# Kernel optimization log

Measured on AMD Instinct MI355X. Metric: run time of the kernel, lower is better.

## Reference

```python
import jax, jax.numpy as jnp
import numpy as np

NUM_HEADS = 16
NEG_INF = -1e18


def setup_inputs() -> dict:
    key = jax.random.key(0)
    ks = jax.random.split(key, 9)
    T, B, D = 2048, 2, 1024
    s = 1.0 / np.sqrt(D)
    return {
        "query": jax.random.normal(ks[0], (T, B, D), jnp.float32),
        "q_w": jax.random.normal(ks[1], (D, D), jnp.float32) * s,
        "q_b": jax.random.normal(ks[2], (D,), jnp.float32) * 0.02,
        "k_w": jax.random.normal(ks[3], (D, D), jnp.float32) * s,
        "k_b": jax.random.normal(ks[4], (D,), jnp.float32) * 0.02,
        "v_w": jax.random.normal(ks[5], (D, D), jnp.float32) * s,
        "v_b": jax.random.normal(ks[6], (D,), jnp.float32) * 0.02,
        "out_w": jax.random.normal(ks[7], (D, D), jnp.float32) * s,
        "out_b": jax.random.normal(ks[8], (D,), jnp.float32) * 0.02,
    }


def reference(query, q_w, q_b, k_w, k_b, v_w, v_b, out_w, out_b):
    # query: [T, B, D] (Time x Batch x Channel). Self-attention, causal mask,
    # dropout=0, need_weights=True.
    T, B, D = query.shape
    H = NUM_HEADS
    hd = D // H
    scaling = 1.0 / jnp.sqrt(jnp.asarray(hd, query.dtype))

    q = (query @ q_w.T + q_b) * scaling
    k = query @ k_w.T + k_b
    v = query @ v_w.T + v_b

    def split_heads(x):  # [T, B, D] -> [B, H, T, hd]
        return x.reshape(T, B, H, hd).transpose(1, 2, 0, 3)

    qh, kh, vh = split_heads(q), split_heads(k), split_heads(v)

    # scores: [B, H, T, T]
    scores = jnp.einsum("bhtd,bhsd->bhts", qh, kh)
    causal = jnp.triu(jnp.full((T, T), NEG_INF, dtype=scores.dtype), k=1)
    scores = scores + causal

    probs = jax.nn.softmax(scores, axis=-1)
    attn = jnp.einsum("bhts,bhsd->bhtd", probs, vh)  # [B, H, T, hd]
    attn = attn.transpose(2, 0, 1, 3).reshape(T, B, D)
    out = attn @ out_w.T + out_b

    # averaged attention weights over heads: [B, T, T]
    avg_weights = probs.sum(axis=1) / H
    return out, avg_weights
```

## Files before the change

### kernel.cpp

```cpp
#include <hip/hip_runtime.h>
#include <hip/hip_bf16.h>
#include <stdint.h>

typedef __hip_bfloat16 bf16;
using short8 = __attribute__((ext_vector_type(8))) short;
using f32x4  = __attribute__((ext_vector_type(4))) float;

#define TDIM 2048
#define BDIM 2
#define DDIM 1024
#define HNUM 16
#define HD   64
#define MDIM 4096
#define M0   16.0f
#define L2E  1.44269504088896f
#define M0B  23.0831207f

__device__ __forceinline__ f32x4 mfma16(short8 a, short8 b, f32x4 c) {
  return __builtin_amdgcn_mfma_f32_16x16x32_bf16(a, b, c, 0, 0, 0);
}

__device__ __forceinline__ float fexp2(float s) {
  return __builtin_amdgcn_exp2f(__builtin_fmaf(s, L2E, -M0B));
}

union S8 { short8 v; bf16 h[8]; };
union P4 { uint2 u; bf16 h[4]; };

__global__ __launch_bounds__(256) void cast_all_kernel(
    const float* __restrict__ q, const float* __restrict__ wq,
    const float* __restrict__ wk, const float* __restrict__ wv,
    const float* __restrict__ wo, bf16* __restrict__ dst) {
  int t4 = blockIdx.x * blockDim.x + threadIdx.x;
  int idx = t4 * 4;
  const float* s;
  if (idx < 4194304)      s = q  + idx;
  else if (idx < 5242880) s = wq + (idx - 4194304);
  else if (idx < 6291456) s = wk + (idx - 5242880);
  else if (idx < 7340032) s = wv + (idx - 6291456);
  else                    s = wo + (idx - 7340032);
  float4 v = *(const float4*)s;
  union { ushort4 u; bf16 b[4]; } pk;
  pk.b[0] = __float2bfloat16(v.x);
  pk.b[1] = __float2bfloat16(v.y);
  pk.b[2] = __float2bfloat16(v.z);
  pk.b[3] = __float2bfloat16(v.w);
  *(ushort4*)(dst + idx) = pk.u;
}

__global__ __launch_bounds__(256, 2) void qkv_kernel(
    const bf16* __restrict__ X, const bf16* __restrict__ Wq,
    const bf16* __restrict__ Wk, const bf16* __restrict__ Wv,
    const float* __restrict__ qb, const float* __restrict__ kb,
    const float* __restrict__ vb, bf16* __restrict__ Qo,
    bf16* __restrict__ Ko, bf16* __restrict__ Vto) {
  __shared__ __align__(16) bf16 Xs[128][72];
  __shared__ __align__(16) bf16 Qs[64][72];
  __shared__ __align__(16) bf16 Ks[64][72];
  __shared__ __align__(16) bf16 Vs[64][72];
  const int tid  = threadIdx.x;
  const int lane = tid & 63, wave = tid >> 6;
  const int m0 = blockIdx.y * 128, n0 = blockIdx.x * 64;
  const int wm = (wave >> 1) * 64, wn = (wave & 1) * 32;
  const int fr = lane & 15, quad = lane >> 4, q8 = quad * 8;
  const int r = tid >> 3, cc = (tid & 7) * 8;
  f32x4 aq[4][2] = {}, ak[4][2] = {}, av[2][4] = {};
  const bf16* xp = X  + (size_t)(m0 + r) * DDIM + cc;
  const bf16* qp = Wq + (size_t)(n0 + r) * DDIM + cc;
  const bf16* kp = Wk + (size_t)(n0 + r) * DDIM + cc;
  const bf16* vp = Wv + (size_t)(n0 + r) * DDIM + cc;
  uint4 xv0, xv1, xv2, xv3, qv0, qv1, kv0, kv1, vv0, vv1;
#define QKV_LD(K0)                                                  \
  do {                                                              \
    xv0 = *(const uint4*)(xp + (K0));                               \
    xv1 = *(const uint4*)(xp + (size_t)32 * DDIM + (K0));           \
    xv2 = *(const uint4*)(xp + (size_t)64 * DDIM + (K0));           \
    xv3 = *(const uint4*)(xp + (size_t)96 * DDIM + (K0));           \
    qv0 = *(const uint4*)(qp + (K0));                               \
    qv1 = *(const uint4*)(qp + (size_t)32 * DDIM + (K0));           \
    kv0 = *(const uint4*)(kp + (K0));                               \
    kv1 = *(const uint4*)(kp + (size_t)32 * DDIM + (K0));           \
    vv0 = *(const uint4*)(vp + (K0));                               \
    vv1 = *(const uint4*)(vp + (size_t)32 * DDIM + (K0));           \
  } while (0)
  QKV_LD(0);
  for (int k0 = 0; k0 < DDIM; k0 += 64) {
    __syncthreads();
    *(uint4*)&Xs[r][cc]      = xv0;
    *(uint4*)&Xs[r + 32][cc] = xv1;
    *(uint4*)&Xs[r + 64][cc] = xv2;
    *(uint4*)&Xs[r + 96][cc] = xv3;
    *(uint4*)&Qs[r][cc]      = qv0;
    *(uint4*)&Qs[r + 32][cc] = qv1;
    *(uint4*)&Ks[r][cc]      = kv0;
    *(uint4*)&Ks[r + 32][cc] = kv1;
    *(uint4*)&Vs[r][cc]      = vv0;
    *(uint4*)&Vs[r + 32][cc] = vv1;
    __syncthreads();
    if (k0 + 64 < DDIM) QKV_LD(k0 + 64);
#pragma unroll
    for (int kk = 0; kk < 2; kk++) {
      const int ko = kk * 32 + q8;
      short8 xf[4], qf[2], kf[2], vf[2];
#pragma unroll
      for (int i = 0; i < 4; i++)
        xf[i] = *(const short8*)&Xs[wm + i * 16 + fr][ko];
#pragma unroll
      for (int j = 0; j < 2; j++) {
        qf[j] = *(const short8*)&Qs[wn + j * 16 + fr][ko];
        kf[j] = *(const short8*)&Ks[wn + j * 16 + fr][ko];
        vf[j] = *(const short8*)&Vs[wn + j * 16 + fr][ko];
      }
#pragma unroll
      for (int i = 0; i < 4; i++)
#pragma unroll
        for (int j = 0; j < 2; j++) {
          aq[i][j] = mfma16(xf[i], qf[j], aq[i][j]);
          ak[i][j] = mfma16(xf[i], kf[j], ak[i][j]);
          av[j][i] = mfma16(vf[j], xf[i], av[j][i]);
        }
    }
  }
#undef QKV_LD
#pragma unroll
  for (int mt = 0; mt < 4; mt++)
#pragma unroll
    for (int nt = 0; nt < 2; nt++)
#pragma unroll
      for (int i = 0; i < 4; i++) {
        int gm = m0 + wm + mt * 16 + quad * 4 + i;
        int gn = n0 + wn + nt * 16 + fr;
        int t = gm >> 1, bb = gm & 1, h = gn >> 6, e = gn & 63;
        size_t o = ((size_t)(bb * HNUM + h) * TDIM + t) * HD + e;
        Qo[o] = __float2bfloat16((aq[mt][nt][i] + qb[gn]) * 0.125f);
        Ko[o] = __float2bfloat16(ak[mt][nt][i] + kb[gn]);
      }
#pragma unroll
  for (int vt = 0; vt < 2; vt++)
#pragma unroll
    for (int xt = 0; xt < 4; xt++)
#pragma unroll
      for (int i = 0; i < 4; i++) {
        int gf = n0 + wn + vt * 16 + quad * 4 + i;
        int gt = m0 + wm + xt * 16 + fr;
        int t = gt >> 1, bb = gt & 1, h = gf >> 6, e = gf & 63;
        Vto[((size_t)(bb * HNUM + h) * HD + e) * TDIM + t] =
            __float2bfloat16(av[vt][xt][i] + vb[gf]);
      }
}

__global__ __launch_bounds__(256) void gemm_out_kernel(
    const bf16* __restrict__ P0, const bf16* __restrict__ P1,
    const bf16* __restrict__ Bw, const float* __restrict__ l0buf,
    const float* __restrict__ l1buf, const float* __restrict__ bias,
    float* __restrict__ of32) {
  __shared__ __align__(16) bf16 As[64][72];
  __shared__ __align__(16) bf16 Bs[64][72];
  __shared__ float sInv[64][16];
  const int tid  = threadIdx.x;
  const int lane = tid & 63, wave = tid >> 6;
  const int m0 = blockIdx.y * 64, n0 = blockIdx.x * 64;
  const int wm = (wave >> 1) * 32, wn = (wave & 1) * 32;
  const int fr = lane & 15, quad = lane >> 4, q8 = quad * 8;
  const int ldr = tid >> 3, ldc = (tid & 7) * 8;
#pragma unroll
  for (int e = 0; e < 4; e++) {
    int idx = tid * 4 + e;
    int row = idx >> 4, h = idx & 15;
    int gm = m0 + row, t = gm >> 1, bb = gm & 1;
    size_t li = (size_t)(bb * HNUM + h) * TDIM + t;
    sInv[row][h] = 1.0f / (l0buf[li] + l1buf[li]);
  }
  f32x4 acc[2][2] = {};
  const size_t ar0 = (size_t)(m0 + ldr) * DDIM + ldc;
  const size_t ar1 = ar0 + (size_t)32 * DDIM;
  const bf16* bp0 = Bw + (size_t)(n0 + ldr) * DDIM + ldc;
  const bf16* bp1 = bp0 + (size_t)32 * DDIM;
  short8 p00v, p10v, p01v, p11v;
  uint4 bv0, bv1;
#define OUT_LD(K0)                                  \
  do {                                              \
    p00v = *(const short8*)&P0[ar0 + (K0)];         \
    p10v = *(const short8*)&P1[ar0 + (K0)];         \
    p01v = *(const short8*)&P0[ar1 + (K0)];         \
    p11v = *(const short8*)&P1[ar1 + (K0)];         \
    bv0  = *(const uint4*)(bp0 + (K0));             \
    bv1  = *(const uint4*)(bp1 + (K0));             \
  } while (0)
  OUT_LD(0);
  __syncthreads();
  for (int k0 = 0; k0 < DDIM; k0 += 64) {
    const float inv0 = sInv[ldr][k0 >> 6];
    const float inv1 = sInv[ldr + 32][k0 >> 6];
    S8 s00, s10, s01, s11, w0, w1;
    s00.v = p00v; s10.v = p10v; s01.v = p01v; s11.v = p11v;
#pragma unroll
    for (int k = 0; k < 8; k++) {
      w0.h[k] = __float2bfloat16(
          (__bfloat162float(s00.h[k]) + __bfloat162float(s10.h[k])) * inv0);
      w1.h[k] = __float2bfloat16(
          (__bfloat162float(s01.h[k]) + __bfloat162float(s11.h[k])) * inv1);
    }
    __syncthreads();
    *(short8*)&As[ldr][ldc]      = w0.v;
    *(short8*)&As[ldr + 32][ldc] = w1.v;
    *(uint4*)&Bs[ldr][ldc]       = bv0;
    *(uint4*)&Bs[ldr + 32][ldc]  = bv1;
    __syncthreads();
    if (k0 + 64 < DDIM) OUT_LD(k0 + 64);
#pragma unroll
    for (int kk = 0; kk < 2; kk++) {
      const int ko = kk * 32 + q8;
      short8 af0, af1, bf0, bf1;
      af0 = *(const short8*)&As[wm + fr][ko];
      af1 = *(const short8*)&As[wm + 16 + fr][ko];
      bf0 = *(const short8*)&Bs[wn + fr][ko];
      bf1 = *(const short8*)&Bs[wn + 16 + fr][ko];
      acc[0][0] = mfma16(af0, bf0, acc[0][0]);
      acc[0][1] = mfma16(af0, bf1, acc[0][1]);
      acc[1][0] = mfma16(af1, bf0, acc[1][0]);
      acc[1][1] = mfma16(af1, bf1, acc[1][1]);
    }
  }
#undef OUT_LD
#pragma unroll
  for (int mt = 0; mt < 2; mt++)
#pragma unroll
    for (int nt = 0; nt < 2; nt++)
#pragma unroll
      for (int i = 0; i < 4; i++) {
        int gm = m0 + wm + mt * 16 + quad * 4 + i;
        int gn = n0 + wn + nt * 16 + fr;
        of32[(size_t)gm * DDIM + gn] = acc[mt][nt][i] + bias[gn];
      }
}

__global__ __launch_bounds__(256) void attn_split_kernel(
    const bf16* __restrict__ Q, const bf16* __restrict__ K,
    const bf16* __restrict__ Vt, bf16* __restrict__ P0o,
    bf16* __restrict__ P1o, float* __restrict__ l0buf,
    float* __restrict__ l1buf) {
  __shared__ __align__(16) bf16 Ks[2][64][40];
  __shared__ __align__(16) bf16 Vs[2][64][40];
  __shared__ __align__(16) bf16 pt[4][32][72];
  const int tid = threadIdx.x, lane = tid & 63, wave = tid >> 6;
  const int bid = blockIdx.x;
  const int part = bid & 1, bh = (bid >> 1) & 31, t128 = 15 - (bid >> 6);
  const int b = bh >> 4, h = bh & 15;
  const int t0 = t128 * 128 + wave * 32;
  const int fr = lane & 15, quad = lane >> 4, q8 = quad * 8;
  const bf16* Qp = Q + ((size_t)bh * TDIM + t0) * HD;
  const bf16* Kp = K + (size_t)bh * TDIM * HD;
  const bf16* Vp = Vt + (size_t)bh * HD * TDIM;
  short8 aq[2][2];
  aq[0][0] = *(const short8*)&Qp[fr * HD + q8];
  aq[0][1] = *(const short8*)&Qp[fr * HD + 32 + q8];
  aq[1][0] = *(const short8*)&Qp[(16 + fr) * HD + q8];
  aq[1][1] = *(const short8*)&Qp[(16 + fr) * HD + 32 + q8];
  const int Cb = 2 * t128 + 2, C0 = t128 + 1;
  const int clo = part ? C0 : 0, chi = part ? Cb : C0;
  const int sr0 = tid >> 3, scc = (tid & 7) * 8, sr1 = sr0 + 32;
  const int ssub = scc >> 5, scol = scc & 31;
  f32x4 oacc[2][4] = {};
  float lsum[2] = {0.f, 0.f};
  uint4 kv0, kv1, vv0, vv1;
  auto ldglob = [&](int c) {
    int s0 = c * 64;
    kv0 = *(const uint4*)&Kp[(size_t)(s0 + sr0) * HD + scc];
    kv1 = *(const uint4*)&Kp[(size_t)(s0 + sr1) * HD + scc];
    vv0 = *(const uint4*)&Vp[(size_t)sr0 * TDIM + s0 + scc];
    vv1 = *(const uint4*)&Vp[(size_t)sr1 * TDIM + s0 + scc];
  };
  ldglob(clo);
  for (int c = clo; c < chi; c++) {
    __syncthreads();
    *(uint4*)&Ks[ssub][sr0][scol] = kv0;
    *(uint4*)&Ks[ssub][sr1][scol] = kv1;
    *(uint4*)&Vs[ssub][sr0][scol] = vv0;
    *(uint4*)&Vs[ssub][sr1][scol] = vv1;
    __syncthreads();
    if (c + 1 < chi) ldglob(c + 1);
    const int s0 = c * 64;
    if (s0 > t0 + 31) continue;
    f32x4 scT[2][4] = {};
#pragma unroll
    for (int j = 0; j < 4; j++) {
      short8 k0f = *(const short8*)&Ks[0][j * 16 + fr][q8];
      short8 k1f = *(const short8*)&Ks[1][j * 16 + fr][q8];
      scT[0][j] = mfma16(k0f, aq[0][0], scT[0][j]);
      scT[0][j] = mfma16(k1f, aq[0][1], scT[0][j]);
      scT[1][j] = mfma16(k0f, aq[1][0], scT[1][j]);
      scT[1][j] = mfma16(k1f, aq[1][1], scT[1][j]);
    }
#pragma unroll
    for (int g = 0; g < 2; g++) {
      const int tg = t0 + g * 16;
#pragma unroll
      for (int j = 0; j < 4; j++) {
        const int sj = s0 + j * 16;
        P4 pk;
        if (sj > tg + 15) {
          pk.u = make_uint2(0u, 0u);
        } else if (sj + 15 <= tg) {
#pragma unroll
          for (int i = 0; i < 4; i++) {
            float p = fexp2(scT[g][j][i]);
            lsum[g] += p;
            pk.h[i] = __float2bfloat16(p);
          }
        } else {
          const int t_row = tg + fr;
          const int s_base = sj + quad * 4;
#pragma unroll
          for (int i = 0; i < 4; i++) {
            float p = 0.f;
            if (s_base + i <= t_row) {
              p = fexp2(scT[g][j][i]);
              lsum[g] += p;
            }
            pk.h[i] = __float2bfloat16(p);
          }
        }
        *(uint2*)&pt[wave][g * 16 + fr][j * 16 + quad * 4] = pk.u;
      }
    }
#pragma unroll
    for (int c2 = 0; c2 < 2; c2++) {
      short8 ap0 = *(const short8*)&pt[wave][fr][c2 * 32 + q8];
      short8 ap1 = *(const short8*)&pt[wave][16 + fr][c2 * 32 + q8];
#pragma unroll
      for (int nt = 0; nt < 4; nt++) {
        short8 vf = *(const short8*)&Vs[c2][nt * 16 + fr][q8];
        oacc[0][nt] = mfma16(ap0, vf, oacc[0][nt]);
        oacc[1][nt] = mfma16(ap1, vf, oacc[1][nt]);
      }
    }
  }
  float lr[2];
#pragma unroll
  for (int g = 0; g < 2; g++) {
    float l = lsum[g];
    l += __shfl_xor(l, 16);
    l += __shfl_xor(l, 32);
    lr[g] = l;
  }
  bf16*  Op = part ? P1o : P0o;
  float* lb = part ? l1buf : l0buf;
#pragma unroll
  for (int g = 0; g < 2; g++)
#pragma unroll
    for (int nt = 0; nt < 4; nt++)
#pragma unroll
      for (int i = 0; i < 4; i++) {
        int t_row = t0 + g * 16 + quad * 4 + i;
        int col = h * HD + nt * 16 + fr;
        Op[((size_t)t_row * BDIM + b) * DDIM + col] =
            __float2bfloat16(oacc[g][nt][i]);
      }
  if (quad == 0) {
    lb[(size_t)bh * TDIM + t0 + fr]      = lr[0];
    lb[(size_t)bh * TDIM + t0 + 16 + fr] = lr[1];
  }
}

__global__ __launch_bounds__(256) void avg_kernel(
    const bf16* __restrict__ Q, const bf16* __restrict__ K,
    const float* __restrict__ l0buf, const float* __restrict__ l1buf,
    float* __restrict__ avgw) {
  const int tid = threadIdx.x;
  int r = blockIdx.x;
  const int b = (r >= 2048) ? 1 : 0;
  r &= 2047;
  float* avp = avgw + (size_t)b * TDIM * TDIM;
  if (r >= 1056) {
    int r2 = r - 1056;
    int ti = 0;
    while (ti < 31 && (ti + 1) * (62 - ti) <= r2) ti++;
    int si = (2 * ti + 2) + (r2 - ti * (63 - ti));
    int t0b = ti * 64, s0 = si * 32;
#pragma unroll
    for (int k = 0; k < 2; k++) {
      int off = (tid * 2 + k) * 4;
      *(float4*)&avp[(size_t)(t0b + (off >> 5)) * TDIM + s0 + (off & 31)] =
          make_float4(0.f, 0.f, 0.f, 0.f);
    }
    return;
  }
  int ti = 0;
  while ((ti + 1) * (ti + 2) <= r) ti++;
  const int si = r - ti * (ti + 1);
  const int t0b = ti * 64, s0 = si * 32;

  __shared__ __align__(16) bf16 Qs[2][64][40];
  __shared__ __align__(16) bf16 Ks2[2][32][40];
  __shared__ float sinvl[HNUM][64];
#pragma unroll
  for (int k = 0; k < 4; k++) {
    int idx = tid + k * 256;
    size_t li = (size_t)(b * HNUM + (idx >> 6)) * TDIM + t0b + (idx & 63);
    sinvl[idx >> 6][idx & 63] = 1.0f / (l0buf[li] + l1buf[li]);
  }
  const int lane = tid & 63, wave = tid >> 6;
  const int fr = lane & 15, quad = lane >> 4, q8 = quad * 8;
  const int twr = wave * 16;
  const int qr0 = tid >> 3, qcc = (tid & 7) * 8, qr1 = qr0 + 32;
  const int qsub = qcc >> 5, qcol = qcc & 31;
  const bf16* Qb = Q + (size_t)b * HNUM * TDIM * HD;
  const bf16* Kb = K + (size_t)b * HNUM * TDIM * HD;
  uint4 qv0, qv1, kv1;
  auto ldh = [&](int hh) {
    const bf16* Qh = Qb + (size_t)hh * TDIM * HD;
    const bf16* Kh = Kb + (size_t)hh * TDIM * HD;
    qv0 = *(const uint4*)&Qh[(size_t)(t0b + qr0) * HD + qcc];
    qv1 = *(const uint4*)&Qh[(size_t)(t0b + qr1) * HD + qcc];
    kv1 = *(const uint4*)&Kh[(size_t)(s0 + (qr0 & 31)) * HD + qcc];
  };
  ldh(0);
  f32x4 facc[2] = {};
  for (int hh = 0; hh < HNUM; hh++) {
    __syncthreads();
    *(uint4*)&Qs[qsub][qr0][qcol] = qv0;
    *(uint4*)&Qs[qsub][qr1][qcol] = qv1;
    if (qr0 < 32) *(uint4*)&Ks2[qsub][qr0][qcol] = kv1;
    else          *(uint4*)&Ks2[qsub][qr0 - 32][qcol] = kv1;
    __syncthreads();
    if (hh + 1 < HNUM) ldh(hh + 1);
    short8 a0 = *(const short8*)&Qs[0][twr + fr][q8];
    short8 a1 = *(const short8*)&Qs[1][twr + fr][q8];
#pragma unroll
    for (int nt = 0; nt < 2; nt++) {
      const int sb = s0 + nt * 16;
      if (sb > t0b + twr + 15) continue;
      short8 b0 = *(const short8*)&Ks2[0][nt * 16 + fr][q8];
      short8 b1 = *(const short8*)&Ks2[1][nt * 16 + fr][q8];
      f32x4 sc = {};
      sc = mfma16(a0, b0, sc);
      sc = mfma16(a1, b1, sc);
      if (sb + 15 <= t0b + twr) {
#pragma unroll
        for (int i = 0; i < 4; i++) {
          int tr = twr + quad * 4 + i;
          facc[nt][i] += fexp2(sc[i]) * sinvl[hh][tr];
        }
      } else {
#pragma unroll
        for (int i = 0; i < 4; i++) {
          int tr = twr + quad * 4 + i;
          if (sb + fr <= t0b + tr)
            facc[nt][i] += fexp2(sc[i]) * sinvl[hh][tr];
        }
      }
    }
  }
#pragma unroll
  for (int nt = 0; nt < 2; nt++)
#pragma unroll
    for (int i = 0; i < 4; i++)
      avp[(size_t)(t0b + twr + quad * 4 + i) * TDIM + s0 + nt * 16 + fr] =
          facc[nt][i] * 0.0625f;
}

extern "C" void kernel_launch(void* const* d_in, const int* in_sizes, int n_in,
                              void* d_out, int out_size, void* d_ws, size_t ws_size,
                              hipStream_t stream) {
  const float* q   = (const float*)d_in[0];
  const float* q_w = (const float*)d_in[1];
  const float* q_b = (const float*)d_in[2];
  const float* k_w = (const float*)d_in[3];
  const float* k_b = (const float*)d_in[4];
  const float* v_w = (const float*)d_in[5];
  const float* v_b = (const float*)d_in[6];
  const float* o_w = (const float*)d_in[7];
  const float* o_b = (const float*)d_in[8];
  float* out = (float*)d_out;
  float* avg = out + (size_t)MDIM * DDIM;

  bf16* ws  = (bf16*)d_ws;
  bf16* Xbf = ws;
  bf16* Wq  = ws + 4194304;
  bf16* Wk  = ws + 5242880;
  bf16* Wv  = ws + 6291456;
  bf16* Wo  = ws + 7340032;
  bf16* Qw  = ws + 8388608;
  bf16* Kw  = ws + 12582912;
  bf16* Vt  = ws + 16777216;
  bf16* P1  = ws + 20971520;
  bf16* P0  = ws;
  float* l0 = (float*)(ws + 4194304);
  float* l1 = (float*)(ws + 4325376);

  cast_all_kernel<<<8192, 256, 0, stream>>>(q, q_w, k_w, v_w, o_w, Xbf);
  qkv_kernel<<<dim3(16, 32), 256, 0, stream>>>(Xbf, Wq, Wk, Wv, q_b, k_b, v_b,
                                               Qw, Kw, Vt);
  attn_split_kernel<<<1024, 256, 0, stream>>>(Qw, Kw, Vt, P0, P1, l0, l1);
  avg_kernel<<<4096, 256, 0, stream>>>(Qw, Kw, l0, l1, avg);
  gemm_out_kernel<<<dim3(16, 64), 256, 0, stream>>>(P0, P1, Wo, l0, l1, o_b, out);
}
```

Measured before the change: 227.2 us.

## Widen avg_kernel tiles to 64x64 and double-buffer Q/K shared memory

The averaged-weights kernel now processes 64x64 score tiles instead of 64x32, halving the block count. Each Q tile load is reused across twice as many key columns, and the block-to-tile mapping is recomputed for the new triangular layout. Q/K shared-memory staging becomes double-buffered with a two-deep register prefetch, so each head needs one barrier instead of two. Shared memory use and register pressure rise, which may lower occupancy.

New measurement: 237.8 us. +4.7%, slower.

```diff
diff --git a/kernel.cpp b/kernel.cpp
--- a/kernel.cpp
+++ b/kernel.cpp
@@ -369,30 +369,31 @@
     float* __restrict__ avgw) {
   const int tid = threadIdx.x;
   int r = blockIdx.x;
-  const int b = (r >= 2048) ? 1 : 0;
-  r &= 2047;
+  const int b = (r >= 1024) ? 1 : 0;
+  r &= 1023;
   float* avp = avgw + (size_t)b * TDIM * TDIM;
-  if (r >= 1056) {
-    int r2 = r - 1056;
+  if (r >= 528) {
+    int r2 = r - 528;
     int ti = 0;
-    while (ti < 31 && (ti + 1) * (62 - ti) <= r2) ti++;
-    int si = (2 * ti + 2) + (r2 - ti * (63 - ti));
-    int t0b = ti * 64, s0 = si * 32;
-#pragma unroll
-    for (int k = 0; k < 2; k++) {
-      int off = (tid * 2 + k) * 4;
-      *(float4*)&avp[(size_t)(t0b + (off >> 5)) * TDIM + s0 + (off & 31)] =
+    while (ti < 31 && 31 * (ti + 1) - (ti + 1) * ti / 2 <= r2) ti++;
+    int si = ti + 1 + (r2 - (31 * ti - ti * (ti - 1) / 2));
+    int t0b = ti * 64, s0 = si * 64;
+#pragma unroll
+    for (int k = 0; k < 4; k++) {
+      int e = tid * 4 + k * 1024;
+      *(float4*)&avp[(size_t)(t0b + (e >> 6)) * TDIM + s0 + (e & 63)] =
           make_float4(0.f, 0.f, 0.f, 0.f);
     }
     return;
   }
   int ti = 0;
-  while ((ti + 1) * (ti + 2) <= r) ti++;
-  const int si = r - ti * (ti + 1);
-  const int t0b = ti * 64, s0 = si * 32;
-
-  __shared__ __align__(16) bf16 Qs[2][64][40];
-  __shared__ __align__(16) bf16 Ks2[2][32][40];
+  while ((ti + 1) * (ti + 2) / 2 <= r) ti++;
+  const int si = r - ti * (ti + 1) / 2;
+  const int t0b = ti * 64, s0 = si * 64;
+  const bool isdiag = (si == ti);
+
+  __shared__ __align__(16) bf16 Qs[2][2][64][40];
+  __shared__ __align__(16) bf16 Ks2[2][2][64][40];
   __shared__ float sinvl[HNUM][64];
 #pragma unroll
   for (int k = 0; k < 4; k++) {
@@ -403,57 +404,64 @@
   const int lane = tid & 63, wave = tid >> 6;
   const int fr = lane & 15, quad = lane >> 4, q8 = quad * 8;
   const int twr = wave * 16;
-  const int qr0 = tid >> 3, qcc = (tid & 7) * 8, qr1 = qr0 + 32;
+  const int qr0 = tid >> 3, qcc = (tid & 7) * 8;
   const int qsub = qcc >> 5, qcol = qcc & 31;
   const bf16* Qb = Q + (size_t)b * HNUM * TDIM * HD;
   const bf16* Kb = K + (size_t)b * HNUM * TDIM * HD;
-  uint4 qv0, qv1, kv1;
-  auto ldh = [&](int hh) {
-    const bf16* Qh = Qb + (size_t)hh * TDIM * HD;
-    const bf16* Kh = Kb + (size_t)hh * TDIM * HD;
-    qv0 = *(const uint4*)&Qh[(size_t)(t0b + qr0) * HD + qcc];
-    qv1 = *(const uint4*)&Qh[(size_t)(t0b + qr1) * HD + qcc];
-    kv1 = *(const uint4*)&Kh[(size_t)(s0 + (qr0 & 31)) * HD + qcc];
-  };
-  ldh(0);
-  f32x4 facc[2] = {};
+  uint4 qv0, qv1, kva, kvb;
+#define AVG_LDH(HH)                                                     \
+  do {                                                                  \
+    const bf16* Qh = Qb + (size_t)(HH) * TDIM * HD;                     \
+    const bf16* Kh = Kb + (size_t)(HH) * TDIM * HD;                     \
+    qv0 = *(const uint4*)&Qh[(size_t)(t0b + qr0) * HD + qcc];           \
+    qv1 = *(const uint4*)&Qh[(size_t)(t0b + qr0 + 32) * HD + qcc];      \
+    kva = *(const uint4*)&Kh[(size_t)(s0 + qr0) * HD + qcc];            \
+    kvb = *(const uint4*)&Kh[(size_t)(s0 + qr0 + 32) * HD + qcc];       \
+  } while (0)
+#define AVG_WR(B)                                                       \
+  do {                                                                  \
+    *(uint4*)&Qs[B][qsub][qr0][qcol]       = qv0;                       \
+    *(uint4*)&Qs[B][qsub][qr0 + 32][qcol]  = qv1;                       \
+    *(uint4*)&Ks2[B][qsub][qr0][qcol]      = kva;                       \
+    *(uint4*)&Ks2[B][qsub][qr0 + 32][qcol] = kvb;                       \
+  } while (0)
+  AVG_LDH(0);
+  AVG_WR(0);
+  AVG_LDH(1);
+  f32x4 facc[4] = {};
+  const int ntlive = isdiag ? wave : 3;
   for (int hh = 0; hh < HNUM; hh++) {
-    __syncthreads();
-    *(uint4*)&Qs[qsub][qr0][qcol] = qv0;
-    *(uint4*)&Qs[qsub][qr1][qcol] = qv1;
-    if (qr0 < 32) *(uint4*)&Ks2[qsub][qr0][qcol] = kv1;
-    else          *(uint4*)&Ks2[qsub][qr0 - 32][qcol] = kv1;
-    __syncthreads();
-    if (hh + 1 < HNUM) ldh(hh + 1);
-    short8 a0 = *(const short8*)&Qs[0][twr + fr][q8];
-    short8 a1 = *(const short8*)&Qs[1][twr + fr][q8];
-#pragma unroll
-    for (int nt = 0; nt < 2; nt++) {
-      const int sb = s0 + nt * 16;
-      if (sb > t0b + twr + 15) continue;
-      short8 b0 = *(const short8*)&Ks2[0][nt * 16 + fr][q8];
-      short8 b1 = *(const short8*)&Ks2[1][nt * 16 + fr][q8];
+    const int cur = hh & 1;
+    __syncthreads();
+    if (hh + 1 < HNUM) AVG_WR(cur ^ 1);
+    if (hh + 2 < HNUM) AVG_LDH(hh + 2);
+    short8 a0 = *(const short8*)&Qs[cur][0][twr + fr][q8];
+    short8 a1 = *(const short8*)&Qs[cur][1][twr + fr][q8];
+#pragma unroll
+    for (int nt = 0; nt < 4; nt++) {
+      if (nt > ntlive) continue;
+      short8 b0 = *(const short8*)&Ks2[cur][0][nt * 16 + fr][q8];
+      short8 b1 = *(const short8*)&Ks2[cur][1][nt * 16 + fr][q8];
       f32x4 sc = {};
       sc = mfma16(a0, b0, sc);
       sc = mfma16(a1, b1, sc);
-      if (sb + 15 <= t0b + twr) {
+      if (isdiag && nt == wave) {
 #pragma unroll
         for (int i = 0; i < 4; i++) {
-          int tr = twr + quad * 4 + i;
-          facc[nt][i] += fexp2(sc[i]) * sinvl[hh][tr];
+          if (fr <= quad * 4 + i)
+            facc[nt][i] += fexp2(sc[i]) * sinvl[hh][twr + quad * 4 + i];
         }
       } else {
 #pragma unroll
-        for (int i = 0; i < 4; i++) {
-          int tr = twr + quad * 4 + i;
-          if (sb + fr <= t0b + tr)
-            facc[nt][i] += fexp2(sc[i]) * sinvl[hh][tr];
-        }
-      }
-    }
-  }
-#pragma unroll
-  for (int nt = 0; nt < 2; nt++)
+        for (int i = 0; i < 4; i++)
+          facc[nt][i] += fexp2(sc[i]) * sinvl[hh][twr + quad * 4 + i];
+      }
+    }
+  }
+#undef AVG_LDH
+#undef AVG_WR
+#pragma unroll
+  for (int nt = 0; nt < 4; nt++)
 #pragma unroll
     for (int i = 0; i < 4; i++)
       avp[(size_t)(t0b + twr + quad * 4 + i) * TDIM + s0 + nt * 16 + fr] =
@@ -493,6 +501,6 @@
   qkv_kernel<<<dim3(16, 32), 256, 0, stream>>>(Xbf, Wq, Wk, Wv, q_b, k_b, v_b,
                                                Qw, Kw, Vt);
   attn_split_kernel<<<1024, 256, 0, stream>>>(Qw, Kw, Vt, P0, P1, l0, l1);
-  avg_kernel<<<4096, 256, 0, stream>>>(Qw, Kw, l0, l1, avg);
+  avg_kernel<<<2048, 256, 0, stream>>>(Qw, Kw, l0, l1, avg);
   gemm_out_kernel<<<dim3(16, 64), 256, 0, stream>>>(P0, P1, Wo, l0, l1, o_b, out);
 }
```
